# Kernel optimization log

Hardware: AMD Instinct MI355X
Metric: run time of the kernel (lower is better)

## Reference

```python
import jax, jax.numpy as jnp
import numpy as np

N = 16384
E = 524288
D_IN, D_HID, D_OUT = 3, 16, 16


def setup_inputs() -> dict:
    key = jax.random.key(0)
    ks = jax.random.split(key, 8)
    node_feats = jax.random.normal(ks[0], (N, D_IN), dtype=jnp.float32)
    edge_idx = jax.random.randint(ks[1], (2, E), 0, N, dtype=jnp.int64)
    # GIN MLP params (Linear(3,16) -> ReLU -> Linear(16,16) -> ReLU), train_eps
    s1 = 1.0 / np.sqrt(D_IN)
    s2 = 1.0 / np.sqrt(D_HID)
    W1 = jax.random.uniform(ks[2], (D_IN, D_HID), jnp.float32, -s1, s1)
    b1 = jax.random.uniform(ks[3], (D_HID,), jnp.float32, -s1, s1)
    W2 = jax.random.uniform(ks[4], (D_HID, D_OUT), jnp.float32, -s2, s2)
    b2 = jax.random.uniform(ks[5], (D_OUT,), jnp.float32, -s2, s2)
    eps = jnp.zeros((), dtype=jnp.float32)  # PyG init eps=0, trainable
    return {"node_feats": node_feats, "edge_idx": edge_idx,
            "W1": W1, "b1": b1, "W2": W2, "b2": b2, "eps": eps}


def reference(node_feats, edge_idx, W1, b1, W2, b2, eps):
    src, tgt = edge_idx[0], edge_idx[1]
    # GIN aggregation: sum of neighbor features via scatter-add over edges
    agg = jax.ops.segment_sum(node_feats[src], tgt, num_segments=N)  # [N, D_IN]
    z = (1.0 + eps) * node_feats + agg
    # 2-layer MLP with ReLU after each linear
    h = jax.nn.relu(z @ W1 + b1)
    h = jax.nn.relu(h @ W2 + b2)  # [N, D_OUT]
    # dense pairwise similarity
    edge_feats = h @ h.T  # [N, N]
    return edge_feats
```

## Files before the change

kernel.cpp:

```cpp
#include <hip/hip_runtime.h>

#define N_NODES 16384
#define N_EDGES 524288
#define TILE_I 128
#define TILE_J 256

typedef float f32x4 __attribute__((ext_vector_type(4)));

__global__ void zero_agg_kernel(float* __restrict__ agg) {
    int i = blockIdx.x * blockDim.x + threadIdx.x;
    if (i < N_NODES * 3) agg[i] = 0.0f;
}

__global__ void scatter_kernel(const int* __restrict__ eidx,
                               const float* __restrict__ x,
                               float* __restrict__ agg) {
    int e = blockIdx.x * blockDim.x + threadIdx.x;
    if (e >= N_EDGES) return;
    int s = eidx[e];
    int t = eidx[N_EDGES + e];
    float f0 = x[s * 3 + 0];
    float f1 = x[s * 3 + 1];
    float f2 = x[s * 3 + 2];
    atomicAdd(&agg[t * 3 + 0], f0);
    atomicAdd(&agg[t * 3 + 1], f1);
    atomicAdd(&agg[t * 3 + 2], f2);
}

__global__ void mlp_kernel(const float* __restrict__ x,
                           const float* __restrict__ agg,
                           const float* __restrict__ W1,
                           const float* __restrict__ b1,
                           const float* __restrict__ W2,
                           const float* __restrict__ b2,
                           const float* __restrict__ eps_p,
                           float* __restrict__ h) {
    int n = blockIdx.x * blockDim.x + threadIdx.x;
    if (n >= N_NODES) return;
    float se = 1.0f + eps_p[0];
    float z0 = se * x[n * 3 + 0] + agg[n * 3 + 0];
    float z1 = se * x[n * 3 + 1] + agg[n * 3 + 1];
    float z2 = se * x[n * 3 + 2] + agg[n * 3 + 2];
    float h1[16];
#pragma unroll
    for (int j = 0; j < 16; ++j) {
        float a = b1[j];
        a += z0 * W1[0 * 16 + j];
        a += z1 * W1[1 * 16 + j];
        a += z2 * W1[2 * 16 + j];
        h1[j] = fmaxf(a, 0.0f);
    }
    float4* h4 = (float4*)&h[n * 16];
#pragma unroll
    for (int oq = 0; oq < 4; ++oq) {
        float4 o;
        float* op = (float*)&o;
#pragma unroll
        for (int c = 0; c < 4; ++c) {
            int oo = oq * 4 + c;
            float a = b2[oo];
#pragma unroll
            for (int j = 0; j < 16; ++j) a += h1[j] * W2[j * 16 + oo];
            op[c] = fmaxf(a, 0.0f);
        }
        h4[oq] = o;
    }
}

__global__ __launch_bounds__(512) void pairwise_kernel(const float* __restrict__ h,
                                                       float* __restrict__ out) {
    __shared__ float hi[TILE_I * 16];
    __shared__ float hjT[16][TILE_J];
    const int i0 = blockIdx.y * TILE_I;
    const int j0 = blockIdx.x * TILE_J;
    const int tid = threadIdx.x;

    const float4* h4 = (const float4*)h;
    float4* hi4 = (float4*)hi;
    hi4[tid] = h4[(size_t)i0 * 4 + tid];
#pragma unroll
    for (int k = 0; k < 2; ++k) {
        int idx = tid + k * 512;
        float4 w = h4[(size_t)j0 * 4 + idx];
        int row = idx >> 2, q = idx & 3;
        hjT[q * 4 + 0][row] = w.x;
        hjT[q * 4 + 1][row] = w.y;
        hjT[q * 4 + 2][row] = w.z;
        hjT[q * 4 + 3][row] = w.w;
    }
    __syncthreads();

    const int tx = tid & 63;
    const int ty = tid >> 6;

    f32x4 hj[16];
#pragma unroll
    for (int k = 0; k < 16; ++k) hj[k] = *(const f32x4*)&hjT[k][tx * 4];

    f32x4* out4 = (f32x4*)out;
    const size_t obase = (size_t)(i0 + ty * 16) * (N_NODES / 4) + (size_t)(j0 >> 2) + tx;

#pragma unroll
    for (int r = 0; r < 16; ++r) {
        const f32x4* hir4 = (const f32x4*)&hi[(ty * 16 + r) * 16];
        f32x4 A0 = hir4[0], A1 = hir4[1], A2 = hir4[2], A3 = hir4[3];
        f32x4 acc = A0.x * hj[0];
        acc += A0.y * hj[1];
        acc += A0.z * hj[2];
        acc += A0.w * hj[3];
        acc += A1.x * hj[4];
        acc += A1.y * hj[5];
        acc += A1.z * hj[6];
        acc += A1.w * hj[7];
        acc += A2.x * hj[8];
        acc += A2.y * hj[9];
        acc += A2.z * hj[10];
        acc += A2.w * hj[11];
        acc += A3.x * hj[12];
        acc += A3.y * hj[13];
        acc += A3.z * hj[14];
        acc += A3.w * hj[15];
        out4[obase + (size_t)r * (N_NODES / 4)] = acc;
    }
}

extern "C" void kernel_launch(void* const* d_in, const int* in_sizes, int n_in,
                              void* d_out, int out_size, void* d_ws, size_t ws_size,
                              hipStream_t stream) {
    const float* node_feats = (const float*)d_in[0];
    const int*   edge_idx   = (const int*)d_in[1];
    const float* W1         = (const float*)d_in[2];
    const float* b1         = (const float*)d_in[3];
    const float* W2         = (const float*)d_in[4];
    const float* b2         = (const float*)d_in[5];
    const float* eps        = (const float*)d_in[6];
    float* out = (float*)d_out;

    float* agg = (float*)d_ws;
    float* h   = (float*)((char*)d_ws + 262144);

    zero_agg_kernel<<<(N_NODES * 3 + 255) / 256, 256, 0, stream>>>(agg);
    scatter_kernel<<<N_EDGES / 256, 256, 0, stream>>>(edge_idx, node_feats, agg);
    mlp_kernel<<<N_NODES / 64, 64, 0, stream>>>(node_feats, agg, W1, b1, W2, b2, eps, h);

    dim3 grid(N_NODES / TILE_J, N_NODES / TILE_I);
    pairwise_kernel<<<grid, 512, 0, stream>>>(h, out);
}
```

Measured before the change: 281.3 us.

## Swizzle pairwise tile order, use nontemporal stores, memset agg, widen MLP blocks

The pairwise kernel moves to a 1D grid with a swizzled block-to-tile mapping that interleaves blocks across eight groups, and writes its output with nontemporal stores to avoid polluting the cache with the 1 GB output. The agg zeroing kernel is replaced by hipMemsetAsync, and the MLP kernel launches with 256 threads per block instead of 64. The main cost targeted is write bandwidth of the large output; the swizzle may change DRAM channel locality in either direction.

```diff
diff --git a/kernel.cpp b/kernel.cpp
--- a/kernel.cpp
+++ b/kernel.cpp
@@ -6,11 +6,6 @@
 #define TILE_J 256
 
 typedef float f32x4 __attribute__((ext_vector_type(4)));
-
-__global__ void zero_agg_kernel(float* __restrict__ agg) {
-    int i = blockIdx.x * blockDim.x + threadIdx.x;
-    if (i < N_NODES * 3) agg[i] = 0.0f;
-}
 
 __global__ void scatter_kernel(const int* __restrict__ eidx,
                                const float* __restrict__ x,
@@ -71,8 +66,10 @@
                                                        float* __restrict__ out) {
     __shared__ float hi[TILE_I * 16];
     __shared__ float hjT[16][TILE_J];
-    const int i0 = blockIdx.y * TILE_I;
-    const int j0 = blockIdx.x * TILE_J;
+    const int flat = blockIdx.x;
+    const int swz = (flat & 7) * 1024 + (flat >> 3);
+    const int i0 = (swz >> 6) * TILE_I;
+    const int j0 = (swz & 63) * TILE_J;
     const int tid = threadIdx.x;
 
     const float4* h4 = (const float4*)h;
@@ -103,24 +100,24 @@
 #pragma unroll
     for (int r = 0; r < 16; ++r) {
         const f32x4* hir4 = (const f32x4*)&hi[(ty * 16 + r) * 16];
-        f32x4 A0 = hir4[0], A1 = hir4[1], A2 = hir4[2], A3 = hir4[3];
-        f32x4 acc = A0.x * hj[0];
-        acc += A0.y * hj[1];
-        acc += A0.z * hj[2];
-        acc += A0.w * hj[3];
-        acc += A1.x * hj[4];
-        acc += A1.y * hj[5];
-        acc += A1.z * hj[6];
-        acc += A1.w * hj[7];
-        acc += A2.x * hj[8];
-        acc += A2.y * hj[9];
-        acc += A2.z * hj[10];
-        acc += A2.w * hj[11];
-        acc += A3.x * hj[12];
-        acc += A3.y * hj[13];
-        acc += A3.z * hj[14];
-        acc += A3.w * hj[15];
-        out4[obase + (size_t)r * (N_NODES / 4)] = acc;
+        f32x4 a0 = hir4[0], a1 = hir4[1], a2 = hir4[2], a3 = hir4[3];
+        f32x4 acc = a0.x * hj[0];
+        acc += a0.y * hj[1];
+        acc += a0.z * hj[2];
+        acc += a0.w * hj[3];
+        acc += a1.x * hj[4];
+        acc += a1.y * hj[5];
+        acc += a1.z * hj[6];
+        acc += a1.w * hj[7];
+        acc += a2.x * hj[8];
+        acc += a2.y * hj[9];
+        acc += a2.z * hj[10];
+        acc += a2.w * hj[11];
+        acc += a3.x * hj[12];
+        acc += a3.y * hj[13];
+        acc += a3.z * hj[14];
+        acc += a3.w * hj[15];
+        __builtin_nontemporal_store(acc, &out4[obase + (size_t)r * (N_NODES / 4)]);
     }
 }
 
@@ -139,10 +136,9 @@
     float* agg = (float*)d_ws;
     float* h   = (float*)((char*)d_ws + 262144);
 
-    zero_agg_kernel<<<(N_NODES * 3 + 255) / 256, 256, 0, stream>>>(agg);
+    hipMemsetAsync(agg, 0, N_NODES * 3 * sizeof(float), stream);
     scatter_kernel<<<N_EDGES / 256, 256, 0, stream>>>(edge_idx, node_feats, agg);
-    mlp_kernel<<<N_NODES / 64, 64, 0, stream>>>(node_feats, agg, W1, b1, W2, b2, eps, h);
+    mlp_kernel<<<N_NODES / 256, 256, 0, stream>>>(node_feats, agg, W1, b1, W2, b2, eps, h);
 
-    dim3 grid(N_NODES / TILE_J, N_NODES / TILE_I);
-    pairwise_kernel<<<grid, 512, 0, stream>>>(h, out);
+    pairwise_kernel<<<8192, 512, 0, stream>>>(h, out);
 }
```

Result: no change. 285.0 us (+1.3%).
